# Optimization experiments

Measured on AMD Instinct MI355X. Metric: run time of the kernel, lower is better.

The kernel has to match this reference:

```python
import jax, jax.numpy as jnp
import numpy as np

N, E, D, Z, EA = 25000, 400000, 32, 128, 4


def _mlp(h, W1, b1, W2, b2):
    # MLP_ALL_ACT: activation after every Linear layer
    h = jax.nn.relu(h @ W1 + b1)
    return jax.nn.relu(h @ W2 + b2)


def _super_edge_conv(x, src, dst, edge_attr,
                     eW1, eb1, eW2, eb2, lW1, lb1, lW2, lb2, residual):
    xi = x[dst]            # [E, F] target node features (PyG x_i)
    xj = x[src]            # [E, F] source node features (PyG x_j)
    d = xj - xi
    p = xj * xi
    e1 = jnp.linalg.norm(d, axis=-1, keepdims=True)   # [E, 1]
    e2 = jnp.sum(p, axis=-1, keepdims=True)           # [E, 1]
    feat = jnp.concatenate([xi, d, p, e1, e2, edge_attr], axis=-1)  # [E, 3F+2+EA]
    m = _mlp(feat, eW1, eb1, eW2, eb2)                # [E, Z]
    agg = jax.ops.segment_max(m, dst, num_segments=x.shape[0])  # max aggr per dst node
    agg = jnp.where(jnp.isfinite(agg), agg, 0.0)      # PyG fills empty segments with 0
    y = _mlp(jnp.concatenate([x, agg], axis=-1), lW1, lb1, lW2, lb2)
    return y + x if residual else y


def setup_inputs() -> dict:
    key = jax.random.key(0)
    keys = iter(jax.random.split(key, 64))

    def xav(din, dout):
        s = float(np.sqrt(2.0 / (din + dout)))
        return jax.random.normal(next(keys), (din, dout), jnp.float32) * s

    inp = {}
    inp["x"] = jax.random.normal(next(keys), (N, D), jnp.float32)
    inp["edge_index"] = jax.random.randint(next(keys), (2, E), 0, N)
    inp["edge_attr"] = jax.random.normal(next(keys), (E, EA), jnp.float32)

    def conv_params(prefix, fin):
        e_in = 3 * fin + 2 + EA
        inp[prefix + "_eW1"] = xav(e_in, Z); inp[prefix + "_eb1"] = jnp.zeros((Z,), jnp.float32)
        inp[prefix + "_eW2"] = xav(Z, Z);    inp[prefix + "_eb2"] = jnp.zeros((Z,), jnp.float32)
        inp[prefix + "_lW1"] = xav(fin + Z, Z); inp[prefix + "_lb1"] = jnp.zeros((Z,), jnp.float32)
        inp[prefix + "_lW2"] = xav(Z, Z);    inp[prefix + "_lb2"] = jnp.zeros((Z,), jnp.float32)

    conv_params("c1", D)
    conv_params("c2", Z)
    conv_params("c3", Z)
    inp["fus_W1"] = xav(3 * Z, 2 * Z); inp["fus_b1"] = jnp.zeros((2 * Z,), jnp.float32)
    inp["fus_W2"] = xav(2 * Z, Z);     inp["fus_b2"] = jnp.zeros((Z,), jnp.float32)
    return inp


def reference(x, edge_index, edge_attr,
              c1_eW1, c1_eb1, c1_eW2, c1_eb2, c1_lW1, c1_lb1, c1_lW2, c1_lb2,
              c2_eW1, c2_eb1, c2_eW2, c2_eb2, c2_lW1, c2_lb1, c2_lW2, c2_lb2,
              c3_eW1, c3_eb1, c3_eW2, c3_eb2, c3_lW1, c3_lb1, c3_lW2, c3_lb2,
              fus_W1, fus_b1, fus_W2, fus_b2):
    src, dst = edge_index[0], edge_index[1]
    x1 = _super_edge_conv(x, src, dst, edge_attr,
                          c1_eW1, c1_eb1, c1_eW2, c1_eb2,
                          c1_lW1, c1_lb1, c1_lW2, c1_lb2, residual=False)
    x2 = _super_edge_conv(x1, src, dst, edge_attr,
                          c2_eW1, c2_eb1, c2_eW2, c2_eb2,
                          c2_lW1, c2_lb1, c2_lW2, c2_lb2, residual=True)
    x3 = _super_edge_conv(x2, src, dst, edge_attr,
                          c3_eW1, c3_eb1, c3_eW2, c3_eb2,
                          c3_lW1, c3_lb1, c3_lW2, c3_lb2, residual=True)
    return _mlp(jnp.concatenate([x1, x2, x3], axis=-1), fus_W1, fus_b1, fus_W2, fus_b2)
```

## Files before the change

kernel.cpp:

```cpp
#include <hip/hip_runtime.h>
#include <math.h>

#define DEV __device__ __forceinline__

typedef __attribute__((ext_vector_type(8))) short bf16x8;
typedef __attribute__((ext_vector_type(4))) float f32x4;

DEV short f2bf(float v) {
    union { float f; unsigned u; } c; c.f = v;
    unsigned r = c.u + 0x7fffu + ((c.u >> 16) & 1u);
    return (short)(r >> 16);
}
DEV float bf2f(short s) {
    return __uint_as_float(((unsigned)(unsigned short)s) << 16);
}
DEV unsigned cvt_pk(float lo, float hi) {
    unsigned r;
    asm("v_cvt_pk_bf16_f32 %0, %1, %2" : "=v"(r) : "v"(lo), "v"(hi));
    return r;
}
DEV uint2 pk4(const float4 v) {
    uint2 r; r.x = cvt_pk(v.x, v.y); r.y = cvt_pk(v.z, v.w); return r;
}

#define NPACK 20
struct PackJobs {
    const float* W[NPACK];
    const float* Wsub[NPACK];
    int KIN[NPACK];
    int NOUT[NPACK];
    int end[NPACK];
};

__global__ __launch_bounds__(256)
void pack_all(PackJobs j, short* __restrict__ out, int total)
{
    const int idx = blockIdx.x * 256 + threadIdx.x;
    if (idx >= total) return;
    int job = 0;
    while (idx >= j.end[job]) ++job;
    const int base = job ? j.end[job - 1] : 0;
    const int w = idx - base;
    const int nout = j.NOUT[job];
    const int per_ks = nout * 32;
    const int ks = w / per_ks;
    const int r  = w - ks * per_ks;
    const int n  = r >> 5;
    const int kg = (r >> 3) & 3;
    const int i  = r & 7;
    const int k  = ks * 32 + kg * 8 + i;
    float val = 0.0f;
    if (k < j.KIN[job]) {
        val = j.W[job][(size_t)k * nout + n];
        if (j.Wsub[job]) val -= j.Wsub[job][(size_t)k * nout + n];
    }
    out[idx] = f2bf(val);
}

__global__ __launch_bounds__(256)
void hist_kernel(const int* __restrict__ dst, int* __restrict__ cnt, int E)
{
    const int e = blockIdx.x * 256 + threadIdx.x;
    if (e < E) atomicAdd(&cnt[dst[e]], 1);
}

__global__ __launch_bounds__(1024)
void scan_kernel(int* __restrict__ cnt, int NB)
{
    __shared__ int part[1024];
    const int t = threadIdx.x;
    const int CH = (NB + 1023) >> 10;
    const int base = t * CH;
    int s = 0;
    for (int k = 0; k < CH; ++k) { const int i = base + k; if (i < NB) s += cnt[i]; }
    part[t] = s;
    __syncthreads();
    for (int off = 1; off < 1024; off <<= 1) {
        const int add = (t >= off) ? part[t - off] : 0;
        __syncthreads();
        part[t] += add;
        __syncthreads();
    }
    int run = part[t] - s;
    for (int k = 0; k < CH; ++k) {
        const int i = base + k;
        if (i < NB) { const int c = cnt[i]; cnt[i] = run; run += c; }
    }
}

__global__ __launch_bounds__(256)
void scatter_kernel(const int* __restrict__ src, const int* __restrict__ dst,
                    const float* __restrict__ ea, int* __restrict__ cursor,
                    int* __restrict__ sSrc, int* __restrict__ sDst,
                    short* __restrict__ eaB, int E)
{
    const int e = blockIdx.x * 256 + threadIdx.x;
    if (e >= E) return;
    const int d = dst[e];
    const int p = atomicAdd(&cursor[d], 1);
    sSrc[p] = src[e];
    sDst[p] = d;
    const float4 a = ((const float4*)ea)[e];
    *(uint2*)(eaB + (size_t)p * 4) = pk4(a);
}

template<int KP, int FSTR, int NOUT, bool BIAS>
DEV void mfma_gemm(const short* aLds, const short* __restrict__ Wpk,
                   const float* __restrict__ b, int row0, int c0, int lane,
                   f32x4 (&acc)[8])
{
    const int l15 = lane & 15;
    const int lg  = lane >> 4;
#pragma unroll
    for (int f = 0; f < 8; ++f) {
        if (BIAS) {
            const float bv = b[c0 + f * 16 + l15];
            acc[f] = (f32x4){bv, bv, bv, bv};
        } else {
            acc[f] = (f32x4){0.f, 0.f, 0.f, 0.f};
        }
    }
    const short* arow  = aLds + (row0 + l15) * FSTR + lg * 8;
    const short* wbase = Wpk + (size_t)(c0 + l15) * 32 + lg * 8;
#pragma unroll
    for (int ks = 0; ks < KP / 32; ++ks) {
        const bf16x8 av = *(const bf16x8*)(arow + ks * 32);
        const short* wp = wbase + (size_t)ks * NOUT * 32;
#pragma unroll
        for (int f = 0; f < 8; ++f) {
            const bf16x8 bv = *(const bf16x8*)(wp + f * 512);
            acc[f] = __builtin_amdgcn_mfma_f32_16x16x32_bf16(av, bv, acc[f], 0, 0, 0);
        }
    }
}

template<int OSTR>
DEV void pack_relu(const f32x4 (&acc)[8], short* out, int row0, int c0, int lane)
{
    const int l15 = lane & 15;
    const int lg  = lane >> 4;
#pragma unroll
    for (int f = 0; f < 8; ++f)
#pragma unroll
        for (int i = 0; i < 4; ++i) {
            const int row = row0 + lg * 4 + i;
            const int col = c0 + f * 16 + l15;
            const float vv = fmaxf(acc[f][i], 0.0f);
            const float o = __shfl_xor(vv, 1);
            if (!(lane & 1))
                *(unsigned*)&out[row * OSTR + col] = cvt_pk(vv, o);
        }
}

DEV void store_bf16(const f32x4 (&acc)[8], short* __restrict__ out,
                    int n0, int wave, int lane, int N)
{
    const int l15 = lane & 15;
    const int lg  = lane >> 4;
#pragma unroll
    for (int f = 0; f < 8; ++f)
#pragma unroll
        for (int i = 0; i < 4; ++i) {
            const float vv = acc[f][i];
            const float o = __shfl_xor(vv, 1);
            if (!(lane & 1)) {
                const int n = n0 + wave * 16 + lg * 4 + i;
                if (n < N)
                    *(unsigned*)&out[(size_t)n * 128 + f * 16 + l15] = cvt_pk(vv, o);
            }
        }
}

template<int FIN, int FSTR>
__global__ __launch_bounds__(256)
void uv_pre(const float* __restrict__ xin,
            const short* __restrict__ Wd, const float* __restrict__ b1,
            const short* __restrict__ Wb,
            short* __restrict__ uB, short* __restrict__ vB,
            float* __restrict__ sq, short* __restrict__ xB, int N)
{
    __shared__ __align__(16) short feat[64 * FSTR];
    const int tid = threadIdx.x, lane = tid & 63, wave = tid >> 6;
    const int n0 = blockIdx.x * 64;
    {
        const int r = tid >> 2, s = tid & 3, n = n0 + r;
        short* frow = feat + r * FSTR;
        if (n < N) {
            const float4* xr = (const float4*)(xin + (size_t)n * FIN);
            float ss = 0.f;
#pragma unroll
            for (int d4 = s; d4 < FIN / 4; d4 += 4) {
                const float4 a = xr[d4];
                ss += a.x * a.x + a.y * a.y + a.z * a.z + a.w * a.w;
                const uint2 sv = pk4(a);
                *(uint2*)(frow + d4 * 4) = sv;
                *(uint2*)(xB + (size_t)n * FIN + d4 * 4) = sv;
            }
            ss += __shfl_xor(ss, 1); ss += __shfl_xor(ss, 2);
            if (s == 0) sq[n] = ss;
        } else {
            for (int d = s * 4; d < FIN; d += 16) *(short4*)(frow + d) = make_short4(0, 0, 0, 0);
        }
    }
    asm volatile("s_waitcnt lgkmcnt(0)" ::: "memory");
    f32x4 acc[8];
    mfma_gemm<FIN, FSTR, 128, true>(feat, Wd, b1, wave * 16, 0, lane, acc);
    store_bf16(acc, uB, n0, wave, lane, N);
    mfma_gemm<FIN, FSTR, 128, false>(feat, Wb, nullptr, wave * 16, 0, lane, acc);
    store_bf16(acc, vB, n0, wave, lane, N);
}

template<int FIN>
__global__ __launch_bounds__(512, 8)
void edge_conv8(const short* __restrict__ xB,
                const int* __restrict__ sSrc, const int* __restrict__ sDst,
                const short* __restrict__ eaB, const float* __restrict__ sq,
                const short* __restrict__ uB, const short* __restrict__ vB,
                const short* __restrict__ W1pk, const short* __restrict__ W2pk,
                const float* __restrict__ b2,
                float* __restrict__ agg, int E, int swzQ, int swzR)
{
    constexpr int KPP  = FIN + 32;
    constexpr int FSTR = KPP + 8;
    constexpr int H1STR = 136;
    constexpr bool MBF = (FSTR >= 132);
    constexpr int MS = MBF ? FSTR : H1STR;
    __shared__ __align__(16) short feat[64 * FSTR];
    __shared__ __align__(16) short h1s[64 * H1STR];
    __shared__ int dstv[64];
    const int tid = threadIdx.x, lane = tid & 63, wave = tid >> 6;
    const int l15 = lane & 15, lg = lane >> 4;
    int bid = blockIdx.x;
    {
        const int xcd = bid & 7, idx = bid >> 3;
        bid = (xcd < swzR ? xcd * (swzQ + 1)
                          : swzR * (swzQ + 1) + (xcd - swzR) * swzQ) + idx;
    }
    const int e0 = bid * 64;
    const int c0 = wave * 16;

    {
        const int r = tid >> 3, s = tid & 7, e = e0 + r;
        short* frow = feat + r * FSTR;
        short* urow = h1s + r * H1STR;
        if (e < E) {
            const int si = sSrc[e], di = sDst[e];
            if (s == 0) dstv[r] = di;
            float sp = 0.f;
#pragma unroll
            for (int c = s; c < FIN / 8; c += 8) {
                const bf16x8 a = *(const bf16x8*)(xB + (size_t)si * FIN + c * 8);
                const bf16x8 b = *(const bf16x8*)(xB + (size_t)di * FIN + c * 8);
                float p[8];
#pragma unroll
                for (int jj = 0; jj < 8; ++jj) {
                    p[jj] = bf2f(a[jj]) * bf2f(b[jj]);
                    sp += p[jj];
                }
                uint4 w;
                w.x = cvt_pk(p[0], p[1]); w.y = cvt_pk(p[2], p[3]);
                w.z = cvt_pk(p[4], p[5]); w.w = cvt_pk(p[6], p[7]);
                *(uint4*)(frow + c * 8) = w;
            }
            sp += __shfl_xor(sp, 1); sp += __shfl_xor(sp, 2); sp += __shfl_xor(sp, 4);
            if (s == 0) {
                const float e1v = sqrtf(fmaxf(sq[si] + sq[di] - 2.f * sp, 0.f));
                *(unsigned*)(frow + FIN) = cvt_pk(e1v, sp);
            }
            if (s == 1) {
                const short4 ea = *(const short4*)(eaB + (size_t)e * 4);
                *(short2*)(frow + FIN + 2) = make_short2(ea.x, ea.y);
                *(short2*)(frow + FIN + 4) = make_short2(ea.z, ea.w);
            }
            for (int d = FIN + 6 + s; d < KPP; d += 8) frow[d] = 0;
#pragma unroll
            for (int c = s; c < 16; c += 8) {
                const bf16x8 uu = *(const bf16x8*)(uB + (size_t)di * 128 + c * 8);
                const bf16x8 vv = *(const bf16x8*)(vB + (size_t)si * 128 + c * 8);
                float o[8];
#pragma unroll
                for (int jj = 0; jj < 8; ++jj)
                    o[jj] = bf2f(uu[jj]) + bf2f(vv[jj]);
                uint4 w;
                w.x = cvt_pk(o[0], o[1]); w.y = cvt_pk(o[2], o[3]);
                w.z = cvt_pk(o[4], o[5]); w.w = cvt_pk(o[6], o[7]);
                *(uint4*)(urow + c * 8) = w;
            }
        } else {
            if (s == 0) dstv[r] = -1;
            for (int d = s * 4; d < KPP; d += 32) *(short4*)(frow + d) = make_short4(0, 0, 0, 0);
            for (int d = s * 4; d < 128; d += 32) *(short4*)(urow + d) = make_short4(0, 0, 0, 0);
        }
    }
    __syncthreads();

    f32x4 acc[4];
#pragma unroll
    for (int sb = 0; sb < 4; ++sb) acc[sb] = (f32x4){0.f, 0.f, 0.f, 0.f};
    {
        const short* wb = W1pk + (size_t)(c0 + l15) * 32 + lg * 8;
#pragma unroll
        for (int ks = 0; ks < KPP / 32; ++ks) {
            const bf16x8 bv = *(const bf16x8*)(wb + (size_t)ks * 4096);
#pragma unroll
            for (int sb = 0; sb < 4; ++sb) {
                const bf16x8 av =
                    *(const bf16x8*)(feat + (sb * 16 + l15) * FSTR + ks * 32 + lg * 8);
                acc[sb] = __builtin_amdgcn_mfma_f32_16x16x32_bf16(av, bv, acc[sb], 0, 0, 0);
            }
        }
    }
#pragma unroll
    for (int sb = 0; sb < 4; ++sb)
#pragma unroll
        for (int i = 0; i < 4; ++i) {
            const int row = sb * 16 + lg * 4 + i;
            const int col = c0 + l15;
            float vv = acc[sb][i] + bf2f(h1s[row * H1STR + col]);
            vv = fmaxf(vv, 0.0f);
            const float o = __shfl_xor(vv, 1);
            if (!(lane & 1))
                *(unsigned*)&h1s[row * H1STR + col] = cvt_pk(vv, o);
        }
    __syncthreads();

    {
        const float bv0 = b2[c0 + l15];
#pragma unroll
        for (int sb = 0; sb < 4; ++sb) acc[sb] = (f32x4){bv0, bv0, bv0, bv0};
    }
    {
        const short* wb = W2pk + (size_t)(c0 + l15) * 32 + lg * 8;
#pragma unroll
        for (int ks = 0; ks < 4; ++ks) {
            const bf16x8 bv = *(const bf16x8*)(wb + (size_t)ks * 4096);
#pragma unroll
            for (int sb = 0; sb < 4; ++sb) {
                const bf16x8 av =
                    *(const bf16x8*)(h1s + (sb * 16 + l15) * H1STR + ks * 32 + lg * 8);
                acc[sb] = __builtin_amdgcn_mfma_f32_16x16x32_bf16(av, bv, acc[sb], 0, 0, 0);
            }
        }
    }
    short* mb = MBF ? feat : h1s;
    if (!MBF) __syncthreads();
#pragma unroll
    for (int sb = 0; sb < 4; ++sb)
#pragma unroll
        for (int i = 0; i < 4; ++i) {
            const int row = sb * 16 + lg * 4 + i;
            const int col = c0 + l15;
            const float vv = fmaxf(acc[sb][i], 0.0f);
            const float o = __shfl_xor(vv, 1);
            if (!(lane & 1))
                *(unsigned*)&mb[row * MS + col] = cvt_pk(vv, o);
        }
    __syncthreads();

    {
        const int c  = tid & 127;
        const int rh = tid >> 7;
        int cur = -1;
        float mx = 0.0f;
#pragma unroll 4
        for (int i2 = 0; i2 < 16; ++i2) {
            const int row = rh * 16 + i2;
            const int d = dstv[row];
            const float val = bf2f(mb[row * MS + c]);
            if (d != cur) {
                if (cur >= 0 && mx > 0.f)
                    atomicMax((int*)agg + (size_t)cur * 128 + c, __float_as_int(mx));
                cur = d;
                mx = val;
            } else {
                mx = fmaxf(mx, val);
            }
        }
        if (cur >= 0 && mx > 0.f)
            atomicMax((int*)agg + (size_t)cur * 128 + c, __float_as_int(mx));
    }
}

template<int FIN, int KP, int FSTR, bool RES>
__global__ __launch_bounds__(256)
void node_uv(const float* __restrict__ xin, const float* __restrict__ agg,
             const short* __restrict__ W1pk, const float* __restrict__ b1,
             const short* __restrict__ W2pk, const float* __restrict__ b2,
             float* __restrict__ out,
             const short* __restrict__ WdN, const float* __restrict__ b1N,
             const short* __restrict__ WbN,
             short* __restrict__ uB, short* __restrict__ vB,
             float* __restrict__ sq, short* __restrict__ xB, int N)
{
    constexpr int H1STR = 136;
    __shared__ __align__(16) short sh[64 * FSTR + 64 * H1STR];
    short* feat = sh;
    short* h1s  = sh + 64 * FSTR;
    const int tid = threadIdx.x, lane = tid & 63, wave = tid >> 6;
    const int l15 = lane & 15, lg = lane >> 4;
    const int n0 = blockIdx.x * 64;

    {
        const int r = tid >> 2, s = tid & 3, n = n0 + r;
        short* frow = feat + r * FSTR;
        if (n < N) {
            const float4* xr = (const float4*)(xin + (size_t)n * FIN);
            const float4* ar = (const float4*)(agg + (size_t)n * 128);
#pragma unroll
            for (int d4 = s; d4 < FIN / 4; d4 += 4)
                *(uint2*)(frow + d4 * 4) = pk4(xr[d4]);
#pragma unroll
            for (int d4 = s; d4 < 32; d4 += 4)
                *(uint2*)(frow + FIN + d4 * 4) = pk4(ar[d4]);
        } else {
            for (int d = s * 4; d < KP; d += 16) *(short4*)(frow + d) = make_short4(0, 0, 0, 0);
        }
    }
    asm volatile("s_waitcnt lgkmcnt(0)" ::: "memory");

    f32x4 acc[8];
    mfma_gemm<KP, FSTR, 128, true>(feat, W1pk, b1, wave * 16, 0, lane, acc);
    pack_relu<H1STR>(acc, h1s, wave * 16, 0, lane);
    asm volatile("s_waitcnt lgkmcnt(0)" ::: "memory");
    mfma_gemm<128, H1STR, 128, true>(h1s, W2pk, b2, wave * 16, 0, lane, acc);

    {
        float ss[4] = {0.f, 0.f, 0.f, 0.f};
#pragma unroll
        for (int f = 0; f < 8; ++f)
#pragma unroll
            for (int i = 0; i < 4; ++i) {
                const int n = n0 + wave * 16 + lg * 4 + i;
                const int c = f * 16 + l15;
                float v = fmaxf(acc[f][i], 0.0f);
                if (RES && n < N) v += xin[(size_t)n * 128 + c];
                if (n < N) out[(size_t)n * 128 + c] = v;
                ss[i] += v * v;
                const float o = __shfl_xor(v, 1);
                if (!(lane & 1)) {
                    const unsigned pk = cvt_pk(v, o);
                    const int row = wave * 16 + lg * 4 + i;
                    *(unsigned*)&h1s[row * H1STR + c] = pk;
                    if (n < N) *(unsigned*)&xB[(size_t)n * 128 + c] = pk;
                }
            }
#pragma unroll
        for (int i = 0; i < 4; ++i) {
            ss[i] += __shfl_xor(ss[i], 1);
            ss[i] += __shfl_xor(ss[i], 2);
            ss[i] += __shfl_xor(ss[i], 4);
            ss[i] += __shfl_xor(ss[i], 8);
            const int n = n0 + wave * 16 + lg * 4 + i;
            if (l15 == 0 && n < N) sq[n] = ss[i];
        }
    }
    asm volatile("s_waitcnt lgkmcnt(0)" ::: "memory");

    mfma_gemm<128, H1STR, 128, true>(h1s, WdN, b1N, wave * 16, 0, lane, acc);
    store_bf16(acc, uB, n0, wave, lane, N);
    mfma_gemm<128, H1STR, 128, false>(h1s, WbN, nullptr, wave * 16, 0, lane, acc);
    store_bf16(acc, vB, n0, wave, lane, N);
}

__global__ __launch_bounds__(128)
void node_fusion(const float* __restrict__ x1, const float* __restrict__ x2,
                 const float* __restrict__ agg,
                 const short* __restrict__ W1pk, const float* __restrict__ b1,
                 const short* __restrict__ W2pk, const float* __restrict__ b2,
                 const short* __restrict__ fW1, const float* __restrict__ fb1,
                 const short* __restrict__ fW2, const float* __restrict__ fb2,
                 float* __restrict__ out, int N)
{
    constexpr int NSTR = 264;
    constexpr int H1N  = 136;
    constexpr int FSF  = 392;
    constexpr int H1F  = 264;
    __shared__ __align__(16) short sh[32 * FSF + 32 * H1F];
    short* featN = sh;
    short* h1N   = sh + 32 * FSF;
    short* featF = sh;
    short* h1F   = sh + 32 * FSF;
    const int tid = threadIdx.x, lane = tid & 63, wave = tid >> 6;
    const int l15 = lane & 15, lg = lane >> 4;
    const int n0 = blockIdx.x * 32;

    {
        const int r = tid >> 2, s = tid & 3, n = n0 + r;
        short* frow = featN + r * NSTR;
        if (n < N) {
            const float4* xr = (const float4*)(x2 + (size_t)n * 128);
            const float4* ar = (const float4*)(agg + (size_t)n * 128);
#pragma unroll
            for (int d4 = s; d4 < 32; d4 += 4) {
                *(uint2*)(frow + d4 * 4)       = pk4(xr[d4]);
                *(uint2*)(frow + 128 + d4 * 4) = pk4(ar[d4]);
            }
        } else {
            for (int d = s * 4; d < 256; d += 16) *(short4*)(frow + d) = make_short4(0, 0, 0, 0);
        }
    }
    asm volatile("s_waitcnt lgkmcnt(0)" ::: "memory");

    f32x4 acc[8];
    mfma_gemm<256, NSTR, 128, true>(featN, W1pk, b1, wave * 16, 0, lane, acc);
    pack_relu<H1N>(acc, h1N, wave * 16, 0, lane);
    asm volatile("s_waitcnt lgkmcnt(0)" ::: "memory");
    mfma_gemm<128, H1N, 128, true>(h1N, W2pk, b2, wave * 16, 0, lane, acc);
#pragma unroll
    for (int f = 0; f < 8; ++f)
#pragma unroll
        for (int i = 0; i < 4; ++i) {
            const int n = n0 + wave * 16 + lg * 4 + i;
            float v = fmaxf(acc[f][i], 0.0f);
            if (n < N) v += x2[(size_t)n * 128 + f * 16 + l15];
            acc[f][i] = v;
        }
    __syncthreads();

    {
        const int r = tid >> 2, s = tid & 3, n = n0 + r;
        short* frow = featF + r * FSF;
        if (n < N) {
            const float4* a1 = (const float4*)(x1 + (size_t)n * 128);
            const float4* a2 = (const float4*)(x2 + (size_t)n * 128);
#pragma unroll
            for (int d4 = s; d4 < 32; d4 += 4) {
                *(uint2*)(frow + d4 * 4)       = pk4(a1[d4]);
                *(uint2*)(frow + 128 + d4 * 4) = pk4(a2[d4]);
            }
        } else {
            for (int d = s * 4; d < 256; d += 16) *(short4*)(frow + d) = make_short4(0, 0, 0, 0);
            for (int d = 256 + s * 4; d < 384; d += 16) *(short4*)(frow + d) = make_short4(0, 0, 0, 0);
        }
    }
#pragma unroll
    for (int f = 0; f < 8; ++f)
#pragma unroll
        for (int i = 0; i < 4; ++i) {
            const int row = wave * 16 + lg * 4 + i;
            const float v = acc[f][i];
            const float o = __shfl_xor(v, 1);
            if (!(lane & 1))
                *(unsigned*)&featF[row * FSF + 256 + f * 16 + l15] = cvt_pk(v, o);
        }
    asm volatile("s_waitcnt lgkmcnt(0)" ::: "memory");

#pragma unroll
    for (int c0 = 0; c0 < 256; c0 += 128) {
        mfma_gemm<384, FSF, 256, true>(featF, fW1, fb1, wave * 16, c0, lane, acc);
        pack_relu<H1F>(acc, h1F, wave * 16, c0, lane);
    }
    asm volatile("s_waitcnt lgkmcnt(0)" ::: "memory");
    mfma_gemm<256, H1F, 128, true>(h1F, fW2, fb2, wave * 16, 0, lane, acc);
#pragma unroll
    for (int f = 0; f < 8; ++f)
#pragma unroll
        for (int i = 0; i < 4; ++i) {
            const int n = n0 + wave * 16 + lg * 4 + i;
            if (n < N)
                out[(size_t)n * 128 + f * 16 + l15] = fmaxf(acc[f][i], 0.0f);
        }
}

extern "C" void kernel_launch(void* const* d_in, const int* in_sizes, int n_in,
                              void* d_out, int out_size, void* d_ws, size_t ws_size,
                              hipStream_t stream)
{
    const float* x    = (const float*)d_in[0];
    const int*   eidx = (const int*)d_in[1];
    const float* ea   = (const float*)d_in[2];

    const float* c1_eW1 = (const float*)d_in[3];
    const float* c1_eb1 = (const float*)d_in[4];
    const float* c1_eW2 = (const float*)d_in[5];
    const float* c1_eb2 = (const float*)d_in[6];
    const float* c1_lW1 = (const float*)d_in[7];
    const float* c1_lb1 = (const float*)d_in[8];
    const float* c1_lW2 = (const float*)d_in[9];
    const float* c1_lb2 = (const float*)d_in[10];

    const float* c2_eW1 = (const float*)d_in[11];
    const float* c2_eb1 = (const float*)d_in[12];
    const float* c2_eW2 = (const float*)d_in[13];
    const float* c2_eb2 = (const float*)d_in[14];
    const float* c2_lW1 = (const float*)d_in[15];
    const float* c2_lb1 = (const float*)d_in[16];
    const float* c2_lW2 = (const float*)d_in[17];
    const float* c2_lb2 = (const float*)d_in[18];

    const float* c3_eW1 = (const float*)d_in[19];
    const float* c3_eb1 = (const float*)d_in[20];
    const float* c3_eW2 = (const float*)d_in[21];
    const float* c3_eb2 = (const float*)d_in[22];
    const float* c3_lW1 = (const float*)d_in[23];
    const float* c3_lb1 = (const float*)d_in[24];
    const float* c3_lW2 = (const float*)d_in[25];
    const float* c3_lb2 = (const float*)d_in[26];

    const float* fus_W1 = (const float*)d_in[27];
    const float* fus_b1 = (const float*)d_in[28];
    const float* fus_W2 = (const float*)d_in[29];
    const float* fus_b2 = (const float*)d_in[30];

    const int N = in_sizes[0] / 32;
    const int E = in_sizes[1] / 2;
    const int* srcI = eidx;
    const int* dstI = eidx + E;

    const size_t NP = (size_t)N * 128;
    float* ws  = (float*)d_ws;
    float* x1  = ws;
    float* x2  = x1 + NP;
    float* agg = x2 + NP;
    float* sq  = agg + NP;
    int* cursor = (int*)(sq + N);
    int* sSrc   = cursor + 25024;
    int* sDst   = sSrc + E;
    short* eaB  = (short*)(sDst + E);
    short* uB   = eaB + (size_t)E * 4;
    short* vB   = uB + NP;
    short* xB   = vB + NP;
    short* wpk  = xB + NP;

    short* e1Wd = wpk + 0;
    short* e1Wb = wpk + 4096;
    short* e1Wp = wpk + 8192;
    short* e1W2 = wpk + 16384;
    short* e2Wd = wpk + 32768;
    short* e2Wb = wpk + 49152;
    short* e2Wp = wpk + 65536;
    short* e2W2 = wpk + 86016;
    short* e3Wd = wpk + 102400;
    short* e3Wb = wpk + 118784;
    short* e3Wp = wpk + 135168;
    short* e3W2 = wpk + 155648;
    short* n1W1 = wpk + 172032;
    short* n1W2 = wpk + 192512;
    short* n2W1 = wpk + 208896;
    short* n2W2 = wpk + 241664;
    short* n3W1 = wpk + 258048;
    short* n3W2 = wpk + 290816;
    short* fW1  = wpk + 307200;
    short* fW2  = wpk + 405504;
    const int packTotal = 438272;

    PackJobs pj;
    const float* pw[NPACK] = {
        c1_eW1, c1_eW1 + 32 * 128, c1_eW1 + 64 * 128, c1_eW2,
        c2_eW1, c2_eW1 + 128 * 128, c2_eW1 + 256 * 128, c2_eW2,
        c3_eW1, c3_eW1 + 128 * 128, c3_eW1 + 256 * 128, c3_eW2,
        c1_lW1, c1_lW2, c2_lW1, c2_lW2, c3_lW1, c3_lW2,
        fus_W1, fus_W2};
    const float* ps[NPACK] = {
        c1_eW1 + 32 * 128, nullptr, nullptr, nullptr,
        c2_eW1 + 128 * 128, nullptr, nullptr, nullptr,
        c3_eW1 + 128 * 128, nullptr, nullptr, nullptr,
        nullptr, nullptr, nullptr, nullptr, nullptr, nullptr,
        nullptr, nullptr};
    const int pk_kin[NPACK]  = {32, 32, 38, 128, 128, 128, 134, 128,
                                128, 128, 134, 128, 160, 128, 256, 128, 256, 128,
                                384, 256};
    const int pk_nout[NPACK] = {128, 128, 128, 128, 128, 128, 128, 128,
                                128, 128, 128, 128, 128, 128, 128, 128, 128, 128,
                                256, 128};
    const int pk_end[NPACK]  = {4096, 8192, 16384, 32768, 49152, 65536, 86016, 102400,
                                118784, 135168, 155648, 172032, 192512, 208896, 241664,
                                258048, 290816, 307200, 405504, 438272};
    for (int i = 0; i < NPACK; ++i) {
        pj.W[i] = pw[i]; pj.Wsub[i] = ps[i];
        pj.KIN[i] = pk_kin[i]; pj.NOUT[i] = pk_nout[i]; pj.end[i] = pk_end[i];
    }
    pack_all<<<(packTotal + 255) / 256, 256, 0, stream>>>(pj, wpk, packTotal);

    const int eblk = (E + 255) / 256;
    hipMemsetAsync(cursor, 0, 25024 * sizeof(int), stream);
    hist_kernel<<<eblk, 256, 0, stream>>>(dstI, cursor, E);
    scan_kernel<<<1, 1024, 0, stream>>>(cursor, N);
    scatter_kernel<<<eblk, 256, 0, stream>>>(srcI, dstI, ea, cursor, sSrc, sDst, eaB, E);

    const int eblocks = (E + 63) / 64;
    const int nblocks = (N + 63) / 64;
    const int fblocks = (N + 31) / 32;
    const int swzQ = eblocks / 8, swzR = eblocks % 8;
    const size_t aggBytes = NP * sizeof(float);

    uv_pre<32, 40><<<nblocks, 256, 0, stream>>>(x, e1Wd, c1_eb1, e1Wb, uB, vB, sq, xB, N);
    hipMemsetAsync(agg, 0, aggBytes, stream);
    edge_conv8<32><<<eblocks, 512, 0, stream>>>(
        xB, sSrc, sDst, eaB, sq, uB, vB, e1Wp, e1W2, c1_eb2, agg, E, swzQ, swzR);
    node_uv<32, 160, 168, false><<<nblocks, 256, 0, stream>>>(
        x, agg, n1W1, c1_lb1, n1W2, c1_lb2, x1,
        e2Wd, c2_eb1, e2Wb, uB, vB, sq, xB, N);

    hipMemsetAsync(agg, 0, aggBytes, stream);
    edge_conv8<128><<<eblocks, 512, 0, stream>>>(
        xB, sSrc, sDst, eaB, sq, uB, vB, e2Wp, e2W2, c2_eb2, agg, E, swzQ, swzR);
    node_uv<128, 256, 264, true><<<nblocks, 256, 0, stream>>>(
        x1, agg, n2W1, c2_lb1, n2W2, c2_lb2, x2,
        e3Wd, c3_eb1, e3Wb, uB, vB, sq, xB, N);

    hipMemsetAsync(agg, 0, aggBytes, stream);
    edge_conv8<128><<<eblocks, 512, 0, stream>>>(
        xB, sSrc, sDst, eaB, sq, uB, vB, e3Wp, e3W2, c3_eb2, agg, E, swzQ, swzR);
    node_fusion<<<fblocks, 128, 0, stream>>>(
        x1, x2, agg, n3W1, c3_lb1, n3W2, c3_lb2,
        fW1, fus_b1, fW2, fus_b2, (float*)d_out, N);
}
```

Before: 515.8 us.

## Fold memsets into kernels and widen node kernels to column-split waves

Removes the separate hipMemsetAsync calls: the cursor is zeroed inside pack_all, and the agg buffer is zeroed inside uv_pre and node_uv after each block has read its own rows. node_uv and node_fusion now run 512 threads per block (node_fusion previously ran 128), with each wave owning a 16-column output slice across all rows instead of a row slice across all columns. This needs extra __syncthreads and a shared reduction for sq, and pads agg to 25024 rows so the zeroing loop never writes past the buffer. The aim is fewer launches and memset passes and more waves per block to hide latency, at the cost of more barriers and repeated loads of the LDS A tiles.

```diff
diff --git a/kernel.cpp b/kernel.cpp
--- a/kernel.cpp
+++ b/kernel.cpp
@@ -33,9 +33,11 @@
 };
 
 __global__ __launch_bounds__(256)
-void pack_all(PackJobs j, short* __restrict__ out, int total)
+void pack_all(PackJobs j, short* __restrict__ out, int total,
+              int* __restrict__ cursor)
 {
     const int idx = blockIdx.x * 256 + threadIdx.x;
+    if (idx < 25024) cursor[idx] = 0;
     if (idx >= total) return;
     int job = 0;
     while (idx >= j.end[job]) ++job;
@@ -134,24 +136,6 @@
     }
 }
 
-template<int OSTR>
-DEV void pack_relu(const f32x4 (&acc)[8], short* out, int row0, int c0, int lane)
-{
-    const int l15 = lane & 15;
-    const int lg  = lane >> 4;
-#pragma unroll
-    for (int f = 0; f < 8; ++f)
-#pragma unroll
-        for (int i = 0; i < 4; ++i) {
-            const int row = row0 + lg * 4 + i;
-            const int col = c0 + f * 16 + l15;
-            const float vv = fmaxf(acc[f][i], 0.0f);
-            const float o = __shfl_xor(vv, 1);
-            if (!(lane & 1))
-                *(unsigned*)&out[row * OSTR + col] = cvt_pk(vv, o);
-        }
-}
-
 DEV void store_bf16(const f32x4 (&acc)[8], short* __restrict__ out,
                     int n0, int wave, int lane, int N)
 {
@@ -177,11 +161,18 @@
             const short* __restrict__ Wd, const float* __restrict__ b1,
             const short* __restrict__ Wb,
             short* __restrict__ uB, short* __restrict__ vB,
-            float* __restrict__ sq, short* __restrict__ xB, int N)
+            float* __restrict__ sq, short* __restrict__ xB,
+            float* __restrict__ aggz, int N)
 {
     __shared__ __align__(16) short feat[64 * FSTR];
     const int tid = threadIdx.x, lane = tid & 63, wave = tid >> 6;
     const int n0 = blockIdx.x * 64;
+    {
+        float4 z = {0.f, 0.f, 0.f, 0.f};
+        float4* ap = (float4*)(aggz + (size_t)n0 * 128);
+#pragma unroll
+        for (int i = 0; i < 8; ++i) ap[tid + i * 256] = z;
+    }
     {
         const int r = tid >> 2, s = tid & 3, n = n0 + r;
         short* frow = feat + r * FSTR;
@@ -382,7 +373,7 @@
 }
 
 template<int FIN, int KP, int FSTR, bool RES>
-__global__ __launch_bounds__(256)
+__global__ __launch_bounds__(512, 4)
 void node_uv(const float* __restrict__ xin, const float* __restrict__ agg,
              const short* __restrict__ W1pk, const float* __restrict__ b1,
              const short* __restrict__ W2pk, const float* __restrict__ b2,
@@ -390,79 +381,181 @@
              const short* __restrict__ WdN, const float* __restrict__ b1N,
              const short* __restrict__ WbN,
              short* __restrict__ uB, short* __restrict__ vB,
-             float* __restrict__ sq, short* __restrict__ xB, int N)
+             float* __restrict__ sq, short* __restrict__ xB,
+             float* __restrict__ aggz, int N)
 {
     constexpr int H1STR = 136;
-    __shared__ __align__(16) short sh[64 * FSTR + 64 * H1STR];
-    short* feat = sh;
-    short* h1s  = sh + 64 * FSTR;
+    __shared__ __align__(16) short feat[64 * FSTR];
+    __shared__ __align__(16) short h1s[64 * H1STR];
+    __shared__ float sqp[8][64];
     const int tid = threadIdx.x, lane = tid & 63, wave = tid >> 6;
     const int l15 = lane & 15, lg = lane >> 4;
     const int n0 = blockIdx.x * 64;
-
-    {
-        const int r = tid >> 2, s = tid & 3, n = n0 + r;
+    const int c0 = wave * 16;
+
+    {
+        const int r = tid >> 3, s = tid & 7, n = n0 + r;
         short* frow = feat + r * FSTR;
         if (n < N) {
             const float4* xr = (const float4*)(xin + (size_t)n * FIN);
             const float4* ar = (const float4*)(agg + (size_t)n * 128);
 #pragma unroll
-            for (int d4 = s; d4 < FIN / 4; d4 += 4)
+            for (int d4 = s; d4 < FIN / 4; d4 += 8)
                 *(uint2*)(frow + d4 * 4) = pk4(xr[d4]);
 #pragma unroll
-            for (int d4 = s; d4 < 32; d4 += 4)
+            for (int d4 = s; d4 < 32; d4 += 8)
                 *(uint2*)(frow + FIN + d4 * 4) = pk4(ar[d4]);
         } else {
-            for (int d = s * 4; d < KP; d += 16) *(short4*)(frow + d) = make_short4(0, 0, 0, 0);
-        }
-    }
-    asm volatile("s_waitcnt lgkmcnt(0)" ::: "memory");
-
-    f32x4 acc[8];
-    mfma_gemm<KP, FSTR, 128, true>(feat, W1pk, b1, wave * 16, 0, lane, acc);
-    pack_relu<H1STR>(acc, h1s, wave * 16, 0, lane);
-    asm volatile("s_waitcnt lgkmcnt(0)" ::: "memory");
-    mfma_gemm<128, H1STR, 128, true>(h1s, W2pk, b2, wave * 16, 0, lane, acc);
-
-    {
-        float ss[4] = {0.f, 0.f, 0.f, 0.f};
-#pragma unroll
-        for (int f = 0; f < 8; ++f)
+            for (int d = s * 4; d < KP; d += 32) *(short4*)(frow + d) = make_short4(0, 0, 0, 0);
+        }
+    }
+    __syncthreads();
+
+    f32x4 acc[4];
+    {
+        const float bv = b1[c0 + l15];
+#pragma unroll
+        for (int sb = 0; sb < 4; ++sb) acc[sb] = (f32x4){bv, bv, bv, bv};
+        const short* wb = W1pk + (size_t)(c0 + l15) * 32 + lg * 8;
+#pragma unroll
+        for (int ks = 0; ks < KP / 32; ++ks) {
+            const bf16x8 bw = *(const bf16x8*)(wb + (size_t)ks * 4096);
+#pragma unroll
+            for (int sb = 0; sb < 4; ++sb) {
+                const bf16x8 av =
+                    *(const bf16x8*)(feat + (sb * 16 + l15) * FSTR + ks * 32 + lg * 8);
+                acc[sb] = __builtin_amdgcn_mfma_f32_16x16x32_bf16(av, bw, acc[sb], 0, 0, 0);
+            }
+        }
+    }
+#pragma unroll
+    for (int sb = 0; sb < 4; ++sb)
+#pragma unroll
+        for (int i = 0; i < 4; ++i) {
+            const int row = sb * 16 + lg * 4 + i;
+            const float vv = fmaxf(acc[sb][i], 0.f);
+            const float o = __shfl_xor(vv, 1);
+            if (!(lane & 1))
+                *(unsigned*)&h1s[row * H1STR + c0 + l15] = cvt_pk(vv, o);
+        }
+    __syncthreads();
+    {
+        const float bv = b2[c0 + l15];
+#pragma unroll
+        for (int sb = 0; sb < 4; ++sb) acc[sb] = (f32x4){bv, bv, bv, bv};
+        const short* wb = W2pk + (size_t)(c0 + l15) * 32 + lg * 8;
+#pragma unroll
+        for (int ks = 0; ks < 4; ++ks) {
+            const bf16x8 bw = *(const bf16x8*)(wb + (size_t)ks * 4096);
+#pragma unroll
+            for (int sb = 0; sb < 4; ++sb) {
+                const bf16x8 av =
+                    *(const bf16x8*)(h1s + (sb * 16 + l15) * H1STR + ks * 32 + lg * 8);
+                acc[sb] = __builtin_amdgcn_mfma_f32_16x16x32_bf16(av, bw, acc[sb], 0, 0, 0);
+            }
+        }
+    }
+#pragma unroll
+    for (int sb = 0; sb < 4; ++sb)
+#pragma unroll
+        for (int i = 0; i < 4; ++i) {
+            const int row = sb * 16 + lg * 4 + i;
+            const int n = n0 + row;
+            const int c = c0 + l15;
+            float v = fmaxf(acc[sb][i], 0.f);
+            if (RES && n < N) v += xin[(size_t)n * 128 + c];
+            acc[sb][i] = v;
+            const float o = __shfl_xor(v, 1);
+            if (!(lane & 1) && n < N) {
+                *(float2*)&out[(size_t)n * 128 + c] = make_float2(v, o);
+                *(unsigned*)&xB[(size_t)n * 128 + c] = cvt_pk(v, o);
+            }
+        }
+    __syncthreads();
+#pragma unroll
+    for (int sb = 0; sb < 4; ++sb)
+#pragma unroll
+        for (int i = 0; i < 4; ++i) {
+            const int row = sb * 16 + lg * 4 + i;
+            const float v = acc[sb][i];
+            const float o = __shfl_xor(v, 1);
+            if (!(lane & 1))
+                *(unsigned*)&h1s[row * H1STR + c0 + l15] = cvt_pk(v, o);
+            float t = v * v;
+            t += __shfl_xor(t, 1); t += __shfl_xor(t, 2);
+            t += __shfl_xor(t, 4); t += __shfl_xor(t, 8);
+            if (l15 == 0) sqp[wave][row] = t;
+        }
+    __syncthreads();
+    if (tid < 64) {
+        const int n = n0 + tid;
+        if (n < N) {
+            float s = 0.f;
+#pragma unroll
+            for (int w = 0; w < 8; ++w) s += sqp[w][tid];
+            sq[n] = s;
+        }
+    }
+    {
+        float4 z = {0.f, 0.f, 0.f, 0.f};
+        float4* ap = (float4*)(aggz + (size_t)n0 * 128);
+#pragma unroll
+        for (int i = 0; i < 4; ++i) ap[tid + i * 512] = z;
+    }
+    {
+        const float bv = b1N[c0 + l15];
+#pragma unroll
+        for (int sb = 0; sb < 4; ++sb) acc[sb] = (f32x4){bv, bv, bv, bv};
+        const short* wb = WdN + (size_t)(c0 + l15) * 32 + lg * 8;
+#pragma unroll
+        for (int ks = 0; ks < 4; ++ks) {
+            const bf16x8 bw = *(const bf16x8*)(wb + (size_t)ks * 4096);
+#pragma unroll
+            for (int sb = 0; sb < 4; ++sb) {
+                const bf16x8 av =
+                    *(const bf16x8*)(h1s + (sb * 16 + l15) * H1STR + ks * 32 + lg * 8);
+                acc[sb] = __builtin_amdgcn_mfma_f32_16x16x32_bf16(av, bw, acc[sb], 0, 0, 0);
+            }
+        }
+#pragma unroll
+        for (int sb = 0; sb < 4; ++sb)
 #pragma unroll
             for (int i = 0; i < 4; ++i) {
-                const int n = n0 + wave * 16 + lg * 4 + i;
-                const int c = f * 16 + l15;
-                float v = fmaxf(acc[f][i], 0.0f);
-                if (RES && n < N) v += xin[(size_t)n * 128 + c];
-                if (n < N) out[(size_t)n * 128 + c] = v;
-                ss[i] += v * v;
+                const int n = n0 + sb * 16 + lg * 4 + i;
+                const float v = acc[sb][i];
                 const float o = __shfl_xor(v, 1);
-                if (!(lane & 1)) {
-                    const unsigned pk = cvt_pk(v, o);
-                    const int row = wave * 16 + lg * 4 + i;
-                    *(unsigned*)&h1s[row * H1STR + c] = pk;
-                    if (n < N) *(unsigned*)&xB[(size_t)n * 128 + c] = pk;
-                }
-            }
-#pragma unroll
-        for (int i = 0; i < 4; ++i) {
-            ss[i] += __shfl_xor(ss[i], 1);
-            ss[i] += __shfl_xor(ss[i], 2);
-            ss[i] += __shfl_xor(ss[i], 4);
-            ss[i] += __shfl_xor(ss[i], 8);
-            const int n = n0 + wave * 16 + lg * 4 + i;
-            if (l15 == 0 && n < N) sq[n] = ss[i];
-        }
-    }
-    asm volatile("s_waitcnt lgkmcnt(0)" ::: "memory");
-
-    mfma_gemm<128, H1STR, 128, true>(h1s, WdN, b1N, wave * 16, 0, lane, acc);
-    store_bf16(acc, uB, n0, wave, lane, N);
-    mfma_gemm<128, H1STR, 128, false>(h1s, WbN, nullptr, wave * 16, 0, lane, acc);
-    store_bf16(acc, vB, n0, wave, lane, N);
-}
-
-__global__ __launch_bounds__(128)
+                if (!(lane & 1) && n < N)
+                    *(unsigned*)&uB[(size_t)n * 128 + c0 + l15] = cvt_pk(v, o);
+            }
+    }
+    {
+#pragma unroll
+        for (int sb = 0; sb < 4; ++sb) acc[sb] = (f32x4){0.f, 0.f, 0.f, 0.f};
+        const short* wb = WbN + (size_t)(c0 + l15) * 32 + lg * 8;
+#pragma unroll
+        for (int ks = 0; ks < 4; ++ks) {
+            const bf16x8 bw = *(const bf16x8*)(wb + (size_t)ks * 4096);
+#pragma unroll
+            for (int sb = 0; sb < 4; ++sb) {
+                const bf16x8 av =
+                    *(const bf16x8*)(h1s + (sb * 16 + l15) * H1STR + ks * 32 + lg * 8);
+                acc[sb] = __builtin_amdgcn_mfma_f32_16x16x32_bf16(av, bw, acc[sb], 0, 0, 0);
+            }
+        }
+#pragma unroll
+        for (int sb = 0; sb < 4; ++sb)
+#pragma unroll
+            for (int i = 0; i < 4; ++i) {
+                const int n = n0 + sb * 16 + lg * 4 + i;
+                const float v = acc[sb][i];
+                const float o = __shfl_xor(v, 1);
+                if (!(lane & 1) && n < N)
+                    *(unsigned*)&vB[(size_t)n * 128 + c0 + l15] = cvt_pk(v, o);
+            }
+    }
+}
+
+__global__ __launch_bounds__(512, 4)
 void node_fusion(const float* __restrict__ x1, const float* __restrict__ x2,
                  const float* __restrict__ agg,
                  const short* __restrict__ W1pk, const float* __restrict__ b1,
@@ -477,88 +570,176 @@
     constexpr int H1F  = 264;
     __shared__ __align__(16) short sh[32 * FSF + 32 * H1F];
     short* featN = sh;
+    short* featF = sh;
     short* h1N   = sh + 32 * FSF;
-    short* featF = sh;
     short* h1F   = sh + 32 * FSF;
     const int tid = threadIdx.x, lane = tid & 63, wave = tid >> 6;
     const int l15 = lane & 15, lg = lane >> 4;
     const int n0 = blockIdx.x * 32;
-
-    {
-        const int r = tid >> 2, s = tid & 3, n = n0 + r;
+    const int c0 = wave * 16;
+
+    {
+        const int r = tid >> 4, s = tid & 15, n = n0 + r;
         short* frow = featN + r * NSTR;
         if (n < N) {
             const float4* xr = (const float4*)(x2 + (size_t)n * 128);
             const float4* ar = (const float4*)(agg + (size_t)n * 128);
 #pragma unroll
-            for (int d4 = s; d4 < 32; d4 += 4) {
+            for (int d4 = s; d4 < 32; d4 += 16) {
                 *(uint2*)(frow + d4 * 4)       = pk4(xr[d4]);
                 *(uint2*)(frow + 128 + d4 * 4) = pk4(ar[d4]);
             }
         } else {
-            for (int d = s * 4; d < 256; d += 16) *(short4*)(frow + d) = make_short4(0, 0, 0, 0);
-        }
-    }
-    asm volatile("s_waitcnt lgkmcnt(0)" ::: "memory");
-
-    f32x4 acc[8];
-    mfma_gemm<256, NSTR, 128, true>(featN, W1pk, b1, wave * 16, 0, lane, acc);
-    pack_relu<H1N>(acc, h1N, wave * 16, 0, lane);
-    asm volatile("s_waitcnt lgkmcnt(0)" ::: "memory");
-    mfma_gemm<128, H1N, 128, true>(h1N, W2pk, b2, wave * 16, 0, lane, acc);
-#pragma unroll
-    for (int f = 0; f < 8; ++f)
-#pragma unroll
-        for (int i = 0; i < 4; ++i) {
-            const int n = n0 + wave * 16 + lg * 4 + i;
-            float v = fmaxf(acc[f][i], 0.0f);
-            if (n < N) v += x2[(size_t)n * 128 + f * 16 + l15];
-            acc[f][i] = v;
-        }
-    __syncthreads();
-
-    {
-        const int r = tid >> 2, s = tid & 3, n = n0 + r;
+            for (int d = s * 4; d < 256; d += 64) *(short4*)(frow + d) = make_short4(0, 0, 0, 0);
+        }
+    }
+    __syncthreads();
+
+    f32x4 acc[2];
+    {
+        const float bv = b1[c0 + l15];
+#pragma unroll
+        for (int sb = 0; sb < 2; ++sb) acc[sb] = (f32x4){bv, bv, bv, bv};
+        const short* wb = W1pk + (size_t)(c0 + l15) * 32 + lg * 8;
+#pragma unroll
+        for (int ks = 0; ks < 8; ++ks) {
+            const bf16x8 bw = *(const bf16x8*)(wb + (size_t)ks * 4096);
+#pragma unroll
+            for (int sb = 0; sb < 2; ++sb) {
+                const bf16x8 av =
+                    *(const bf16x8*)(featN + (sb * 16 + l15) * NSTR + ks * 32 + lg * 8);
+                acc[sb] = __builtin_amdgcn_mfma_f32_16x16x32_bf16(av, bw, acc[sb], 0, 0, 0);
+            }
+        }
+    }
+#pragma unroll
+    for (int sb = 0; sb < 2; ++sb)
+#pragma unroll
+        for (int i = 0; i < 4; ++i) {
+            const int row = sb * 16 + lg * 4 + i;
+            const float vv = fmaxf(acc[sb][i], 0.f);
+            const float o = __shfl_xor(vv, 1);
+            if (!(lane & 1))
+                *(unsigned*)&h1N[row * H1N + c0 + l15] = cvt_pk(vv, o);
+        }
+    __syncthreads();
+    {
+        const float bv = b2[c0 + l15];
+#pragma unroll
+        for (int sb = 0; sb < 2; ++sb) acc[sb] = (f32x4){bv, bv, bv, bv};
+        const short* wb = W2pk + (size_t)(c0 + l15) * 32 + lg * 8;
+#pragma unroll
+        for (int ks = 0; ks < 4; ++ks) {
+            const bf16x8 bw = *(const bf16x8*)(wb + (size_t)ks * 4096);
+#pragma unroll
+            for (int sb = 0; sb < 2; ++sb) {
+                const bf16x8 av =
+                    *(const bf16x8*)(h1N + (sb * 16 + l15) * H1N + ks * 32 + lg * 8);
+                acc[sb] = __builtin_amdgcn_mfma_f32_16x16x32_bf16(av, bw, acc[sb], 0, 0, 0);
+            }
+        }
+    }
+#pragma unroll
+    for (int sb = 0; sb < 2; ++sb)
+#pragma unroll
+        for (int i = 0; i < 4; ++i) {
+            const int n = n0 + sb * 16 + lg * 4 + i;
+            float v = fmaxf(acc[sb][i], 0.f);
+            if (n < N) v += x2[(size_t)n * 128 + c0 + l15];
+            acc[sb][i] = v;
+        }
+    __syncthreads();
+
+    {
+        const int r = tid >> 4, s = tid & 15, n = n0 + r;
         short* frow = featF + r * FSF;
         if (n < N) {
             const float4* a1 = (const float4*)(x1 + (size_t)n * 128);
             const float4* a2 = (const float4*)(x2 + (size_t)n * 128);
 #pragma unroll
-            for (int d4 = s; d4 < 32; d4 += 4) {
+            for (int d4 = s; d4 < 32; d4 += 16) {
                 *(uint2*)(frow + d4 * 4)       = pk4(a1[d4]);
                 *(uint2*)(frow + 128 + d4 * 4) = pk4(a2[d4]);
             }
         } else {
-            for (int d = s * 4; d < 256; d += 16) *(short4*)(frow + d) = make_short4(0, 0, 0, 0);
-            for (int d = 256 + s * 4; d < 384; d += 16) *(short4*)(frow + d) = make_short4(0, 0, 0, 0);
-        }
-    }
-#pragma unroll
-    for (int f = 0; f < 8; ++f)
-#pragma unroll
-        for (int i = 0; i < 4; ++i) {
-            const int row = wave * 16 + lg * 4 + i;
-            const float v = acc[f][i];
+            for (int d = s * 4; d < 384; d += 64) *(short4*)(frow + d) = make_short4(0, 0, 0, 0);
+        }
+    }
+#pragma unroll
+    for (int sb = 0; sb < 2; ++sb)
+#pragma unroll
+        for (int i = 0; i < 4; ++i) {
+            const int row = sb * 16 + lg * 4 + i;
+            const float v = acc[sb][i];
             const float o = __shfl_xor(v, 1);
             if (!(lane & 1))
-                *(unsigned*)&featF[row * FSF + 256 + f * 16 + l15] = cvt_pk(v, o);
-        }
-    asm volatile("s_waitcnt lgkmcnt(0)" ::: "memory");
-
-#pragma unroll
-    for (int c0 = 0; c0 < 256; c0 += 128) {
-        mfma_gemm<384, FSF, 256, true>(featF, fW1, fb1, wave * 16, c0, lane, acc);
-        pack_relu<H1F>(acc, h1F, wave * 16, c0, lane);
-    }
-    asm volatile("s_waitcnt lgkmcnt(0)" ::: "memory");
-    mfma_gemm<256, H1F, 128, true>(h1F, fW2, fb2, wave * 16, 0, lane, acc);
-#pragma unroll
-    for (int f = 0; f < 8; ++f)
-#pragma unroll
-        for (int i = 0; i < 4; ++i) {
-            const int n = n0 + wave * 16 + lg * 4 + i;
-            if (n < N)
-                out[(size_t)n * 128 + f * 16 + l15] = fmaxf(acc[f][i], 0.0f);
+                *(unsigned*)&featF[row * FSF + 256 + c0 + l15] = cvt_pk(v, o);
+        }
+    __syncthreads();
+
+    {
+        const int cc0 = wave * 32;
+        f32x4 a2[2][2];
+#pragma unroll
+        for (int f = 0; f < 2; ++f) {
+            const float bv = fb1[cc0 + f * 16 + l15];
+            a2[0][f] = (f32x4){bv, bv, bv, bv};
+            a2[1][f] = (f32x4){bv, bv, bv, bv};
+        }
+        const short* wb = fW1 + (size_t)(cc0 + l15) * 32 + lg * 8;
+#pragma unroll
+        for (int ks = 0; ks < 12; ++ks) {
+            const short* wp = wb + (size_t)ks * 8192;
+            const bf16x8 bv0 = *(const bf16x8*)(wp);
+            const bf16x8 bv1 = *(const bf16x8*)(wp + 512);
+#pragma unroll
+            for (int sb = 0; sb < 2; ++sb) {
+                const bf16x8 av =
+                    *(const bf16x8*)(featF + (sb * 16 + l15) * FSF + ks * 32 + lg * 8);
+                a2[sb][0] = __builtin_amdgcn_mfma_f32_16x16x32_bf16(av, bv0, a2[sb][0], 0, 0, 0);
+                a2[sb][1] = __builtin_amdgcn_mfma_f32_16x16x32_bf16(av, bv1, a2[sb][1], 0, 0, 0);
+            }
+        }
+#pragma unroll
+        for (int sb = 0; sb < 2; ++sb)
+#pragma unroll
+            for (int f = 0; f < 2; ++f)
+#pragma unroll
+                for (int i = 0; i < 4; ++i) {
+                    const int row = sb * 16 + lg * 4 + i;
+                    const int col = cc0 + f * 16 + l15;
+                    const float vv = fmaxf(a2[sb][f][i], 0.f);
+                    const float o = __shfl_xor(vv, 1);
+                    if (!(lane & 1))
+                        *(unsigned*)&h1F[row * H1F + col] = cvt_pk(vv, o);
+                }
+    }
+    __syncthreads();
+    {
+        const float bv = fb2[c0 + l15];
+#pragma unroll
+        for (int sb = 0; sb < 2; ++sb) acc[sb] = (f32x4){bv, bv, bv, bv};
+        const short* wb = fW2 + (size_t)(c0 + l15) * 32 + lg * 8;
+#pragma unroll
+        for (int ks = 0; ks < 8; ++ks) {
+            const bf16x8 bw = *(const bf16x8*)(wb + (size_t)ks * 4096);
+#pragma unroll
+            for (int sb = 0; sb < 2; ++sb) {
+                const bf16x8 av =
+                    *(const bf16x8*)(h1F + (sb * 16 + l15) * H1F + ks * 32 + lg * 8);
+                acc[sb] = __builtin_amdgcn_mfma_f32_16x16x32_bf16(av, bw, acc[sb], 0, 0, 0);
+            }
+        }
+    }
+#pragma unroll
+    for (int sb = 0; sb < 2; ++sb)
+#pragma unroll
+        for (int i = 0; i < 4; ++i) {
+            const int n = n0 + sb * 16 + lg * 4 + i;
+            const float v = fmaxf(acc[sb][i], 0.f);
+            const float o = __shfl_xor(v, 1);
+            if (!(lane & 1) && n < N)
+                *(float2*)&out[(size_t)n * 128 + c0 + l15] = make_float2(v, o);
         }
 }
 
@@ -607,13 +788,14 @@
     const int* srcI = eidx;
     const int* dstI = eidx + E;
 
-    const size_t NP = (size_t)N * 128;
+    const size_t NP  = (size_t)N * 128;
+    const size_t NPA = (size_t)25024 * 128;
     float* ws  = (float*)d_ws;
     float* x1  = ws;
     float* x2  = x1 + NP;
     float* agg = x2 + NP;
-    float* sq  = agg + NP;
-    int* cursor = (int*)(sq + N);
+    float* sq  = agg + NPA;
+    int* cursor = (int*)(sq + 25024);
     int* sSrc   = cursor + 25024;
     int* sDst   = sSrc + E;
     short* eaB  = (short*)(sDst + E);
@@ -670,10 +852,9 @@
         pj.W[i] = pw[i]; pj.Wsub[i] = ps[i];
         pj.KIN[i] = pk_kin[i]; pj.NOUT[i] = pk_nout[i]; pj.end[i] = pk_end[i];
     }
-    pack_all<<<(packTotal + 255) / 256, 256, 0, stream>>>(pj, wpk, packTotal);
+    pack_all<<<(packTotal + 255) / 256, 256, 0, stream>>>(pj, wpk, packTotal, cursor);
 
     const int eblk = (E + 255) / 256;
-    hipMemsetAsync(cursor, 0, 25024 * sizeof(int), stream);
     hist_kernel<<<eblk, 256, 0, stream>>>(dstI, cursor, E);
     scan_kernel<<<1, 1024, 0, stream>>>(cursor, N);
     scatter_kernel<<<eblk, 256, 0, stream>>>(srcI, dstI, ea, cursor, sSrc, sDst, eaB, E);
@@ -682,27 +863,24 @@
     const int nblocks = (N + 63) / 64;
     const int fblocks = (N + 31) / 32;
     const int swzQ = eblocks / 8, swzR = eblocks % 8;
-    const size_t aggBytes = NP * sizeof(float);
-
-    uv_pre<32, 40><<<nblocks, 256, 0, stream>>>(x, e1Wd, c1_eb1, e1Wb, uB, vB, sq, xB, N);
-    hipMemsetAsync(agg, 0, aggBytes, stream);
+
+    uv_pre<32, 40><<<nblocks, 256, 0, stream>>>(
+        x, e1Wd, c1_eb1, e1Wb, uB, vB, sq, xB, agg, N);
     edge_conv8<32><<<eblocks, 512, 0, stream>>>(
         xB, sSrc, sDst, eaB, sq, uB, vB, e1Wp, e1W2, c1_eb2, agg, E, swzQ, swzR);
-    node_uv<32, 160, 168, false><<<nblocks, 256, 0, stream>>>(
+    node_uv<32, 160, 168, false><<<nblocks, 512, 0, stream>>>(
         x, agg, n1W1, c1_lb1, n1W2, c1_lb2, x1,
-        e2Wd, c2_eb1, e2Wb, uB, vB, sq, xB, N);
-
-    hipMemsetAsync(agg, 0, aggBytes, stream);
+        e2Wd, c2_eb1, e2Wb, uB, vB, sq, xB, agg, N);
+
     edge_conv8<128><<<eblocks, 512, 0, stream>>>(
         xB, sSrc, sDst, eaB, sq, uB, vB, e2Wp, e2W2, c2_eb2, agg, E, swzQ, swzR);
-    node_uv<128, 256, 264, true><<<nblocks, 256, 0, stream>>>(
+    node_uv<128, 256, 264, true><<<nblocks, 512, 0, stream>>>(
         x1, agg, n2W1, c2_lb1, n2W2, c2_lb2, x2,
-        e3Wd, c3_eb1, e3Wb, uB, vB, sq, xB, N);
-
-    hipMemsetAsync(agg, 0, aggBytes, stream);
+        e3Wd, c3_eb1, e3Wb, uB, vB, sq, xB, agg, N);
+
     edge_conv8<128><<<eblocks, 512, 0, stream>>>(
         xB, sSrc, sDst, eaB, sq, uB, vB, e3Wp, e3W2, c3_eb2, agg, E, swzQ, swzR);
-    node_fusion<<<fblocks, 128, 0, stream>>>(
+    node_fusion<<<fblocks, 512, 0, stream>>>(
         x1, x2, agg, n3W1, c3_lb1, n3W2, c3_lb2,
         fW1, fus_b1, fW2, fus_b2, (float*)d_out, N);
 }
```

New measurement: 421.3 us. -18.3%, faster.
